# Kernel tuning notes

Measured on AMD Instinct MI355X. Metric: run time of the kernel, lower is better.

## Reference

```python
import jax, jax.numpy as jnp
import numpy as np

B, TT, TP, TO = 8, 128, 256, 512
V, D, H, L = 1024, 1024, 16, 12
FF = 4 * D
DH = D // H
EPS = 1e-5


def _pe(t, d):
    # sinusoidal PE: concat(sin(omega*t), cos(omega*t)), omega = exp(-ln(1e4)*i/(d/2))
    half = d // 2
    omega = jnp.exp(-jnp.log(10000.0) * jnp.arange(half, dtype=jnp.float32) / half)
    ang = jnp.arange(t, dtype=jnp.float32)[:, None] * omega[None, :]  # (t, d/2)
    return jnp.concatenate([jnp.sin(ang), jnp.cos(ang)], axis=-1)  # (t, d)


def _ln(x, g, b):
    mu = x.mean(axis=-1, keepdims=True)
    var = ((x - mu) ** 2).mean(axis=-1, keepdims=True)
    return (x - mu) / jnp.sqrt(var + EPS) * g + b


def _forward(text_ids, prompt_ids, output_ids, text_tab, prompt_tab, output_tab, sep,
             ln1_g, ln1_b, qkv_w, out_w, out_b, ln2_g, ln2_b,
             ff1_w, ff1_b, ff2_w, ff2_b, fc_w, fc_b):
    emb = lambda ids, tab: tab[ids] + _pe(ids.shape[1], D)[None]
    sep_tok = jnp.broadcast_to(sep, (B, 1, D))
    # join: [text, sep, prompt, sep, output]
    x = jnp.concatenate([emb(text_ids, text_tab), sep_tok,
                         emb(prompt_ids, prompt_tab), sep_tok,
                         emb(output_ids, output_tab)], axis=1)  # (B, T, D)
    T = x.shape[1]
    causal = jnp.tril(jnp.ones((T, T), dtype=bool))  # (T, T)
    scale = DH ** -0.5
    neg = -jnp.finfo(x.dtype).max
    for l in range(L):
        # attention block (prenorm residual); uniform lengths -> mask m is all ones
        h = _ln(x, ln1_g[l], ln1_b[l])
        qkv = h @ qkv_w[l]  # (B, T, 3D)
        q, k, v = jnp.split(qkv, 3, axis=-1)
        q = q.reshape(B, T, H, DH)
        k = k.reshape(B, T, H, DH)
        v = v.reshape(B, T, H, DH)
        e = jnp.einsum('bihd,bjhd->bijh', q, k) * scale
        e = jnp.where(causal[None, :, :, None], e, neg)
        a = jax.nn.softmax(e, axis=2)
        o = jnp.einsum('bijh,bjhd->bihd', a, v).reshape(B, T, D)
        x = x + o @ out_w[l] + out_b[l]
        # ffn block (prenorm residual), exact GELU as torch nn.GELU default
        h2 = _ln(x, ln2_g[l], ln2_b[l])
        ff = jax.nn.gelu(h2 @ ff1_w[l] + ff1_b[l], approximate=False) @ ff2_w[l] + ff2_b[l]
        x = x + ff
    h = x @ fc_w + fc_b  # (B, T, V)
    return h[:, -1, :]  # logits of last position, (B, V)


def setup_inputs() -> dict:
    key = jax.random.key(0)
    ks = iter(jax.random.split(key, 32))
    s = 0.02
    inp = {
        'text_ids': jax.random.randint(next(ks), (B, TT), 0, V),
        'prompt_ids': jax.random.randint(next(ks), (B, TP), 0, V),
        'output_ids': jax.random.randint(next(ks), (B, TO), 0, V),
        'text_tab': jax.random.normal(next(ks), (V, D), jnp.float32) * s,
        'prompt_tab': jax.random.normal(next(ks), (V, D), jnp.float32) * s,
        'output_tab': jax.random.normal(next(ks), (V, D), jnp.float32) * s,
        'sep': jax.random.normal(next(ks), (D,), jnp.float32),
        'ln1_g': jnp.ones((L, D), jnp.float32),
        'ln1_b': jnp.zeros((L, D), jnp.float32),
        'qkv_w': jax.random.normal(next(ks), (L, D, 3 * D), jnp.float32) * s,
        'out_w': jax.random.normal(next(ks), (L, D, D), jnp.float32) * s,
        'out_b': jnp.zeros((L, D), jnp.float32),
        'ln2_g': jnp.ones((L, D), jnp.float32),
        'ln2_b': jnp.zeros((L, D), jnp.float32),
        'ff1_w': jax.random.normal(next(ks), (L, D, FF), jnp.float32) * s,
        'ff1_b': jnp.zeros((L, FF), jnp.float32),
        'ff2_w': jax.random.normal(next(ks), (L, FF, D), jnp.float32) * s,
        'ff2_b': jnp.zeros((L, D), jnp.float32),
        'fc_w': jax.random.normal(next(ks), (D, V), jnp.float32) * s,
        'fc_b': jnp.zeros((V,), jnp.float32),
    }
    return inp


def reference(text_ids, prompt_ids, output_ids, text_tab, prompt_tab, output_tab, sep,
              ln1_g, ln1_b, qkv_w, out_w, out_b, ln2_g, ln2_b,
              ff1_w, ff1_b, ff2_w, ff2_b, fc_w, fc_b):
    return _forward(text_ids, prompt_ids, output_ids, text_tab, prompt_tab, output_tab, sep,
                    ln1_g, ln1_b, qkv_w, out_w, out_b, ln2_g, ln2_b,
                    ff1_w, ff1_b, ff2_w, ff2_b, fc_w, fc_b)
```

## Files before the change

### kernel.cpp

```cpp
#include <hip/hip_runtime.h>
#include <hip/hip_bf16.h>
#include <math.h>

#define Bn 8
#define Tn 898
#define Dn 1024
#define Hn 16
#define DHn 64
#define Ln 12
#define FFn 4096
#define Vn 1024
#define BT (Bn*Tn)

typedef short bf16x8 __attribute__((ext_vector_type(8)));
typedef float f32x4 __attribute__((ext_vector_type(4)));

__device__ __forceinline__ ushort f2bf(float f) {
    union { float f; unsigned u; } c; c.f = f;
    unsigned r = c.u + 0x7fffu + ((c.u >> 16) & 1u);
    return (ushort)(r >> 16);
}

__device__ __forceinline__ void glds16(const void* g, void* l) {
    __builtin_amdgcn_global_load_lds(
        (const __attribute__((address_space(1))) unsigned int*)g,
        (__attribute__((address_space(3))) unsigned int*)l, 16, 0, 0);
}

__global__ __launch_bounds__(256) void transpose_cast_kernel(
    const float* __restrict__ in, ushort* __restrict__ out,
    int K, int N, size_t in_ls, size_t out_ls)
{
    __shared__ ushort t[64][68];
    const float* inp = in + (size_t)blockIdx.z * in_ls;
    ushort* outp = out + (size_t)blockIdx.z * out_ls;
    int n0 = blockIdx.x * 64, k0 = blockIdx.y * 64;
    int tx = threadIdx.x & 63, ty = threadIdx.x >> 6;
    #pragma unroll
    for (int p = 0; p < 16; p++) {
        int kl = p * 4 + ty;
        t[tx][kl] = f2bf(inp[(size_t)(k0 + kl) * N + n0 + tx]);
    }
    __syncthreads();
    int tx4 = threadIdx.x & 15, ty4 = threadIdx.x >> 4;
    #pragma unroll
    for (int p = 0; p < 4; p++) {
        int nl = p * 16 + ty4;
        ushort4 v;
        v.x = t[nl][4*tx4]; v.y = t[nl][4*tx4+1]; v.z = t[nl][4*tx4+2]; v.w = t[nl][4*tx4+3];
        *(ushort4*)&outp[(size_t)(n0 + nl) * K + k0 + 4*tx4] = v;
    }
}

__global__ __launch_bounds__(256) void embed_kernel(
    const int* __restrict__ tids, const int* __restrict__ pids, const int* __restrict__ oids,
    const float* __restrict__ ttab, const float* __restrict__ ptab, const float* __restrict__ otab,
    const float* __restrict__ sep, float* __restrict__ x)
{
    int bp = blockIdx.x;
    int b = bp / Tn, pos = bp - b * Tn;
    int d0 = threadIdx.x * 4;
    float4 r;
    if (pos == 128 || pos == 385) {
        r = *(const float4*)(sep + d0);
    } else {
        int t; int id; const float* tab;
        if (pos < 128)      { t = pos;       id = tids[b*128 + t]; tab = ttab; }
        else if (pos < 385) { t = pos - 129; id = pids[b*256 + t]; tab = ptab; }
        else                { t = pos - 386; id = oids[b*512 + t]; tab = otab; }
        float4 e = *(const float4*)(tab + (size_t)id * Dn + d0);
        float pe[4];
        #pragma unroll
        for (int i = 0; i < 4; i++) {
            int d = d0 + i;
            int ii = d & 511;
            float omega = expf(-9.210340371976184f * (float)ii * (1.0f/512.0f));
            float ang = (float)t * omega;
            pe[i] = (d < 512) ? sinf(ang) : cosf(ang);
        }
        r.x = e.x + pe[0]; r.y = e.y + pe[1]; r.z = e.z + pe[2]; r.w = e.w + pe[3];
    }
    *(float4*)(x + (size_t)bp * Dn + d0) = r;
}

__global__ __launch_bounds__(256) void ln_kernel(
    const float* __restrict__ x, const float* __restrict__ g, const float* __restrict__ bt,
    ushort* __restrict__ out)
{
    __shared__ float red[8];
    int row = blockIdx.x, tid = threadIdx.x;
    float4 v = ((const float4*)(x + (size_t)row * Dn))[tid];
    float s = v.x + v.y + v.z + v.w;
    #pragma unroll
    for (int o = 32; o; o >>= 1) s += __shfl_down(s, o);
    if ((tid & 63) == 0) red[tid >> 6] = s;
    __syncthreads();
    float mu = (red[0] + red[1] + red[2] + red[3]) * (1.0f / Dn);
    float d0 = v.x - mu, d1 = v.y - mu, d2 = v.z - mu, d3 = v.w - mu;
    float s2 = d0*d0 + d1*d1 + d2*d2 + d3*d3;
    #pragma unroll
    for (int o = 32; o; o >>= 1) s2 += __shfl_down(s2, o);
    if ((tid & 63) == 0) red[4 + (tid >> 6)] = s2;
    __syncthreads();
    float var = (red[4] + red[5] + red[6] + red[7]) * (1.0f / Dn);
    float rstd = rsqrtf(var + 1e-5f);
    float4 gg = ((const float4*)g)[tid];
    float4 bb = ((const float4*)bt)[tid];
    ushort4 o4;
    o4.x = f2bf(d0 * rstd * gg.x + bb.x);
    o4.y = f2bf(d1 * rstd * gg.y + bb.y);
    o4.z = f2bf(d2 * rstd * gg.z + bb.z);
    o4.w = f2bf(d3 * rstd * gg.w + bb.w);
    ((ushort4*)(out + (size_t)row * Dn))[tid] = o4;
}

template<int BN, int MODE>
__global__ __launch_bounds__(256) void gemmk(
    const ushort* __restrict__ A, const ushort* __restrict__ Bw,
    const float* __restrict__ bias, const float* __restrict__ resid,
    void* __restrict__ Cout, int M, int N, int K, int nx)
{
    constexpr int NI = BN / 32;
    __shared__ ushort sA[128 * 32];
    __shared__ ushort sB[BN * 32];

    int tid = threadIdx.x, lane = tid & 63, wv = tid >> 6;
    int wm = wv >> 1, wn = wv & 1;
    int l16 = lane & 15, lhi = lane >> 4;

    int nb = gridDim.x, bid = blockIdx.x;
    int qq = nb >> 3, rr8 = nb & 7;
    int xcd = bid & 7, idx = bid >> 3;
    int wg = (xcd < rr8 ? xcd * (qq + 1) : rr8 * (qq + 1) + (xcd - rr8) * qq) + idx;
    int mt = wg / nx, ntt = wg - mt * nx;
    int m0 = mt * 128, n0 = ntt * BN;

    f32x4 acc[4][NI];
    #pragma unroll
    for (int i = 0; i < 4; i++)
        #pragma unroll
        for (int j = 0; j < NI; j++) acc[i][j] = (f32x4){0.f, 0.f, 0.f, 0.f};

    const size_t K2 = (size_t)K * 2;
    int srow = lane >> 2;
    int schk = ((lane & 3) ^ ((lane >> 3) & 3)) * 16;
    const char* Abase = (const char*)A + (size_t)m0 * K2 + schk;
    const char* Bbase = (const char*)Bw + (size_t)n0 * K2 + schk;

    auto stage = [&](int t) {
        size_t ko = (size_t)t * 64;
        glds16(Abase + (size_t)(wv * 16 + srow) * K2 + ko,       (char*)sA + wv * 1024);
        glds16(Abase + (size_t)((wv + 4) * 16 + srow) * K2 + ko, (char*)sA + (wv + 4) * 1024);
        glds16(Bbase + (size_t)(wv * 16 + srow) * K2 + ko,       (char*)sB + wv * 1024);
        if (BN == 128)
            glds16(Bbase + (size_t)((wv + 4) * 16 + srow) * K2 + ko, (char*)sB + (wv + 4) * 1024);
    };

    const int sc = (lhi ^ ((l16 >> 1) & 3)) * 8;
    auto compute = [&]() {
        bf16x8 af[4], bf[NI];
        #pragma unroll
        for (int mi = 0; mi < 4; mi++)
            af[mi] = *(const bf16x8*)&sA[(wm * 64 + mi * 16 + l16) * 32 + sc];
        #pragma unroll
        for (int ni = 0; ni < NI; ni++)
            bf[ni] = *(const bf16x8*)&sB[(wn * (16 * NI) + ni * 16 + l16) * 32 + sc];
        #pragma unroll
        for (int mi = 0; mi < 4; mi++)
            #pragma unroll
            for (int ni = 0; ni < NI; ni++)
                acc[mi][ni] = __builtin_amdgcn_mfma_f32_16x16x32_bf16(af[mi], bf[ni], acc[mi][ni], 0, 0, 0);
    };

    int ntile = K >> 5;
    for (int t = 0; t < ntile; ++t) {
        __syncthreads();
        stage(t);
        __syncthreads();
        compute();
    }

    #pragma unroll
    for (int mi = 0; mi < 4; mi++) {
        int rl = wm * 64 + mi * 16 + lhi * 4;
        #pragma unroll
        for (int ni = 0; ni < NI; ni++) {
            int gcol = n0 + wn * (16 * NI) + ni * 16 + l16;
            float bs = (MODE == 0) ? 0.0f : bias[gcol];
            #pragma unroll
            for (int j = 0; j < 4; j++) {
                int grow = m0 + rl + j;
                if (grow >= M) continue;
                float v = acc[mi][ni][j] + bs;
                if (MODE == 1) {
                    float rv = resid[(size_t)grow * N + gcol];
                    ((float*)Cout)[(size_t)grow * N + gcol] = rv + v;
                } else if (MODE == 2) {
                    float u = v * (1.5957691216f + 0.0713548163f * v * v);
                    float g = v / (1.0f + __expf(-u));
                    ((ushort*)Cout)[(size_t)grow * N + gcol] = f2bf(g);
                } else {
                    ((ushort*)Cout)[(size_t)grow * N + gcol] = f2bf(v);
                }
            }
        }
    }
}

__global__ __launch_bounds__(256) void attn_kernel(
    const ushort* __restrict__ qkv, ushort* __restrict__ out)
{
    __shared__ ushort Ksm[64 * 72];
    __shared__ ushort Vsm[64 * 72];
    __shared__ ushort Psm[4][16 * 72];
    int qt = blockIdx.x, b = blockIdx.y, h = blockIdx.z;
    int tid = threadIdx.x, lane = tid & 63, wave = tid >> 6;
    int l16 = lane & 15, lhi = lane >> 4;

    int qrow = qt*64 + wave*16 + l16;
    bf16x8 qf0 = {}, qf1 = {};
    if (qrow < Tn) {
        const ushort* qp = qkv + (size_t)(b*Tn + qrow) * 3072 + h*64 + lhi*8;
        qf0 = *(const bf16x8*)qp;
        qf1 = *(const bf16x8*)(qp + 32);
    }

    f32x4 o[4];
    #pragma unroll
    for (int i = 0; i < 4; i++) o[i] = (f32x4){0.f,0.f,0.f,0.f};
    float mrun[4] = {-1e30f,-1e30f,-1e30f,-1e30f};
    float sume[4] = {0.f,0.f,0.f,0.f};

    int kr = tid >> 2, cc = (tid & 3) * 16;
    const ushort* kvbase = qkv + (size_t)(b*Tn) * 3072 + h*64 + cc;
    int qg = qt*64 + wave*16 + lhi*4;

    for (int jt = 0; jt <= qt; jt++) {
        int kvr = jt*64 + kr;
        uint4 k0 = make_uint4(0,0,0,0), k1 = k0, v0 = k0, v1 = k0;
        if (kvr < Tn) {
            const ushort* p = kvbase + (size_t)kvr * 3072;
            k0 = *(const uint4*)(p + 1024);
            k1 = *(const uint4*)(p + 1024 + 8);
            v0 = *(const uint4*)(p + 2048);
            v1 = *(const uint4*)(p + 2048 + 8);
        }
        __syncthreads();
        *(uint4*)&Ksm[kr * 72 + cc] = k0;
        *(uint4*)&Ksm[kr * 72 + cc + 8] = k1;
        {
            ushort vv[16];
            *(uint4*)&vv[0] = v0; *(uint4*)&vv[8] = v1;
            #pragma unroll
            for (int i = 0; i < 16; i++) Vsm[(cc + i) * 72 + kr] = vv[i];
        }
        __syncthreads();

        f32x4 s[4];
        #pragma unroll
        for (int ni = 0; ni < 4; ni++) {
            s[ni] = (f32x4){0.f,0.f,0.f,0.f};
            bf16x8 kf0 = *(const bf16x8*)&Ksm[(ni*16 + l16) * 72 + lhi*8];
            bf16x8 kf1 = *(const bf16x8*)&Ksm[(ni*16 + l16) * 72 + lhi*8 + 32];
            s[ni] = __builtin_amdgcn_mfma_f32_16x16x32_bf16(qf0, kf0, s[ni], 0, 0, 0);
            s[ni] = __builtin_amdgcn_mfma_f32_16x16x32_bf16(qf1, kf1, s[ni], 0, 0, 0);
        }

        float pv[4][4];
        #pragma unroll
        for (int j = 0; j < 4; j++) {
            int qgj = qg + j;
            float mx = -1e30f;
            #pragma unroll
            for (int ni = 0; ni < 4; ni++) {
                int kvg = jt*64 + ni*16 + l16;
                float e = (kvg <= qgj && kvg < Tn) ? s[ni][j] * 0.125f : -1e30f;
                pv[ni][j] = e;
                mx = fmaxf(mx, e);
            }
            #pragma unroll
            for (int m = 1; m < 16; m <<= 1) mx = fmaxf(mx, __shfl_xor(mx, m));
            float mnew = fmaxf(mrun[j], mx);
            float fac = expf(mrun[j] - mnew);
            mrun[j] = mnew;
            float rs = 0.f;
            #pragma unroll
            for (int ni = 0; ni < 4; ni++) { pv[ni][j] = expf(pv[ni][j] - mnew); rs += pv[ni][j]; }
            #pragma unroll
            for (int m = 1; m < 16; m <<= 1) rs += __shfl_xor(rs, m);
            sume[j] = sume[j] * fac + rs;
            #pragma unroll
            for (int di = 0; di < 4; di++) o[di][j] *= fac;
        }

        #pragma unroll
        for (int j = 0; j < 4; j++)
            #pragma unroll
            for (int ni = 0; ni < 4; ni++)
                Psm[wave][(lhi*4 + j) * 72 + ni*16 + l16] = f2bf(pv[ni][j]);
        __syncthreads();

        bf16x8 pf0 = *(const bf16x8*)&Psm[wave][l16 * 72 + lhi*8];
        bf16x8 pf1 = *(const bf16x8*)&Psm[wave][l16 * 72 + lhi*8 + 32];
        #pragma unroll
        for (int di = 0; di < 4; di++) {
            bf16x8 vf0 = *(const bf16x8*)&Vsm[(di*16 + l16) * 72 + lhi*8];
            bf16x8 vf1 = *(const bf16x8*)&Vsm[(di*16 + l16) * 72 + lhi*8 + 32];
            o[di] = __builtin_amdgcn_mfma_f32_16x16x32_bf16(pf0, vf0, o[di], 0, 0, 0);
            o[di] = __builtin_amdgcn_mfma_f32_16x16x32_bf16(pf1, vf1, o[di], 0, 0, 0);
        }
    }

    #pragma unroll
    for (int j = 0; j < 4; j++) {
        int qgj = qg + j;
        if (qgj >= Tn) continue;
        float inv = 1.0f / sume[j];
        #pragma unroll
        for (int di = 0; di < 4; di++)
            out[(size_t)(b*Tn + qgj) * Dn + h*64 + di*16 + l16] = f2bf(o[di][j] * inv);
    }
}

__global__ __launch_bounds__(256) void fc_kernel(
    const float* __restrict__ x, const float* __restrict__ w,
    const float* __restrict__ bias, float* __restrict__ out)
{
    __shared__ float xs[Dn];
    int b = blockIdx.y;
    int v = blockIdx.x * 256 + threadIdx.x;
    float4 t = ((const float4*)(x + (size_t)(b*Tn + Tn - 1) * Dn))[threadIdx.x];
    ((float4*)xs)[threadIdx.x] = t;
    __syncthreads();
    float acc = bias[v];
    for (int d = 0; d < Dn; d++)
        acc = fmaf(xs[d], w[(size_t)d * Vn + v], acc);
    out[(size_t)b * Vn + v] = acc;
}

extern "C" void kernel_launch(void* const* d_in, const int* in_sizes, int n_in,
                              void* d_out, int out_size, void* d_ws, size_t ws_size,
                              hipStream_t stream)
{
    const int*   text_ids  = (const int*)d_in[0];
    const int*   prompt_ids= (const int*)d_in[1];
    const int*   output_ids= (const int*)d_in[2];
    const float* text_tab  = (const float*)d_in[3];
    const float* prompt_tab= (const float*)d_in[4];
    const float* output_tab= (const float*)d_in[5];
    const float* sep       = (const float*)d_in[6];
    const float* ln1_g     = (const float*)d_in[7];
    const float* ln1_b     = (const float*)d_in[8];
    const float* qkv_w     = (const float*)d_in[9];
    const float* out_w     = (const float*)d_in[10];
    const float* out_b     = (const float*)d_in[11];
    const float* ln2_g     = (const float*)d_in[12];
    const float* ln2_b     = (const float*)d_in[13];
    const float* ff1_w     = (const float*)d_in[14];
    const float* ff1_b     = (const float*)d_in[15];
    const float* ff2_w     = (const float*)d_in[16];
    const float* ff2_b     = (const float*)d_in[17];
    const float* fc_w      = (const float*)d_in[18];
    const float* fc_b      = (const float*)d_in[19];

    char* ws = (char*)d_ws;
    float*  x    = (float*)(ws);
    ushort* h    = (ushort*)(ws + 29425664);
    ushort* qkv  = (ushort*)(ws + 44630016);
    ushort* attn = (ushort*)(ws + 90243072);
    ushort* ff1o = (ushort*)(ws + 105447424);
    ushort* wT   = (ushort*)(ws + 166264832);

    const size_t L_STRIDE = 12582912;
    const size_t OFF_QKV = 0, OFF_OUT = 3145728, OFF_FF1 = 4194304, OFF_FF2 = 8388608;
    const size_t upfront_need = 166264832ULL + 2ULL * L_STRIDE * Ln;
    const bool upfront = ws_size >= upfront_need;

    if (upfront) {
        transpose_cast_kernel<<<dim3(48,16,Ln), 256, 0, stream>>>(qkv_w, wT + OFF_QKV, Dn, 3*Dn, (size_t)Dn*3*Dn, L_STRIDE);
        transpose_cast_kernel<<<dim3(16,16,Ln), 256, 0, stream>>>(out_w, wT + OFF_OUT, Dn, Dn,   (size_t)Dn*Dn,   L_STRIDE);
        transpose_cast_kernel<<<dim3(64,16,Ln), 256, 0, stream>>>(ff1_w, wT + OFF_FF1, Dn, FFn,  (size_t)Dn*FFn,  L_STRIDE);
        transpose_cast_kernel<<<dim3(16,64,Ln), 256, 0, stream>>>(ff2_w, wT + OFF_FF2, FFn, Dn,  (size_t)FFn*Dn,  L_STRIDE);
    }

    embed_kernel<<<BT, 256, 0, stream>>>(text_ids, prompt_ids, output_ids,
                                         text_tab, prompt_tab, output_tab, sep, x);

    for (int l = 0; l < Ln; l++) {
        ushort* wb = upfront ? (wT + (size_t)l * L_STRIDE) : wT;
        if (!upfront) {
            transpose_cast_kernel<<<dim3(48,16,1), 256, 0, stream>>>(qkv_w + (size_t)l*Dn*3*Dn, wb + OFF_QKV, Dn, 3*Dn, 0, 0);
            transpose_cast_kernel<<<dim3(16,16,1), 256, 0, stream>>>(out_w + (size_t)l*Dn*Dn,   wb + OFF_OUT, Dn, Dn,   0, 0);
            transpose_cast_kernel<<<dim3(64,16,1), 256, 0, stream>>>(ff1_w + (size_t)l*Dn*FFn,  wb + OFF_FF1, Dn, FFn,  0, 0);
            transpose_cast_kernel<<<dim3(16,64,1), 256, 0, stream>>>(ff2_w + (size_t)l*FFn*Dn,  wb + OFF_FF2, FFn, Dn,  0, 0);
        }
        ln_kernel<<<BT, 256, 0, stream>>>(x, ln1_g + l*Dn, ln1_b + l*Dn, h);
        gemmk<128,0><<<57*24, 256, 0, stream>>>(
            h, wb + OFF_QKV, nullptr, nullptr, qkv, BT, 3*Dn, Dn, 24);
        attn_kernel<<<dim3(15, Bn, Hn), 256, 0, stream>>>(qkv, attn);
        gemmk<64,1><<<57*16, 256, 0, stream>>>(
            attn, wb + OFF_OUT, out_b + l*Dn, x, x, BT, Dn, Dn, 16);
        ln_kernel<<<BT, 256, 0, stream>>>(x, ln2_g + l*Dn, ln2_b + l*Dn, h);
        gemmk<128,2><<<57*32, 256, 0, stream>>>(
            h, wb + OFF_FF1, ff1_b + l*FFn, nullptr, ff1o, BT, FFn, Dn, 32);
        gemmk<64,1><<<57*16, 256, 0, stream>>>(
            ff1o, wb + OFF_FF2, ff2_b + l*Dn, x, x, BT, Dn, FFn, 16);
    }

    fc_kernel<<<dim3(Vn/256, Bn), 256, 0, stream>>>(x, fc_w, fc_b, (float*)d_out);
}
```

Measured before the change: 5.360 ms.

## Double-buffer GEMM LDS staging and use one wavefront per row in layernorm

The GEMM now keeps two LDS buffers and issues the global-to-LDS loads for the next K-tile before computing the current one. This replaces two barriers per tile with a single vmcnt wait plus barrier, so load latency can overlap MFMA work, at the cost of twice the shared memory per block. The layernorm kernel now gives each row to one 64-lane wavefront and reduces with xor shuffles, which removes the shared-memory reductions and block barriers and launches a quarter as many blocks. BT is divisible by 4, so all rows are still covered.

```diff
diff --git a/kernel.cpp b/kernel.cpp
--- a/kernel.cpp
+++ b/kernel.cpp
@@ -26,6 +26,9 @@
         (const __attribute__((address_space(1))) unsigned int*)g,
         (__attribute__((address_space(3))) unsigned int*)l, 16, 0, 0);
 }
+
+#define BARRIER() __builtin_amdgcn_s_barrier()
+#define VMCNT0() asm volatile("s_waitcnt vmcnt(0)" ::: "memory")
 
 __global__ __launch_bounds__(256) void transpose_cast_kernel(
     const float* __restrict__ in, ushort* __restrict__ out,
@@ -87,31 +90,40 @@
     const float* __restrict__ x, const float* __restrict__ g, const float* __restrict__ bt,
     ushort* __restrict__ out)
 {
-    __shared__ float red[8];
-    int row = blockIdx.x, tid = threadIdx.x;
-    float4 v = ((const float4*)(x + (size_t)row * Dn))[tid];
-    float s = v.x + v.y + v.z + v.w;
-    #pragma unroll
-    for (int o = 32; o; o >>= 1) s += __shfl_down(s, o);
-    if ((tid & 63) == 0) red[tid >> 6] = s;
-    __syncthreads();
-    float mu = (red[0] + red[1] + red[2] + red[3]) * (1.0f / Dn);
-    float d0 = v.x - mu, d1 = v.y - mu, d2 = v.z - mu, d3 = v.w - mu;
-    float s2 = d0*d0 + d1*d1 + d2*d2 + d3*d3;
-    #pragma unroll
-    for (int o = 32; o; o >>= 1) s2 += __shfl_down(s2, o);
-    if ((tid & 63) == 0) red[4 + (tid >> 6)] = s2;
-    __syncthreads();
-    float var = (red[4] + red[5] + red[6] + red[7]) * (1.0f / Dn);
-    float rstd = rsqrtf(var + 1e-5f);
-    float4 gg = ((const float4*)g)[tid];
-    float4 bb = ((const float4*)bt)[tid];
-    ushort4 o4;
-    o4.x = f2bf(d0 * rstd * gg.x + bb.x);
-    o4.y = f2bf(d1 * rstd * gg.y + bb.y);
-    o4.z = f2bf(d2 * rstd * gg.z + bb.z);
-    o4.w = f2bf(d3 * rstd * gg.w + bb.w);
-    ((ushort4*)(out + (size_t)row * Dn))[tid] = o4;
+    int row = blockIdx.x * 4 + (threadIdx.x >> 6);
+    int lane = threadIdx.x & 63;
+    const float4* xr = (const float4*)(x + (size_t)row * Dn);
+    float4 v[4];
+    float s = 0.f;
+    #pragma unroll
+    for (int i = 0; i < 4; i++) {
+        v[i] = xr[lane + 64 * i];
+        s += v[i].x + v[i].y + v[i].z + v[i].w;
+    }
+    #pragma unroll
+    for (int o = 32; o; o >>= 1) s += __shfl_xor(s, o);
+    float mu = s * (1.0f / Dn);
+    float s2 = 0.f;
+    #pragma unroll
+    for (int i = 0; i < 4; i++) {
+        v[i].x -= mu; v[i].y -= mu; v[i].z -= mu; v[i].w -= mu;
+        s2 += v[i].x*v[i].x + v[i].y*v[i].y + v[i].z*v[i].z + v[i].w*v[i].w;
+    }
+    #pragma unroll
+    for (int o = 32; o; o >>= 1) s2 += __shfl_xor(s2, o);
+    float rstd = rsqrtf(s2 * (1.0f / Dn) + 1e-5f);
+    ushort4* orow = (ushort4*)(out + (size_t)row * Dn);
+    #pragma unroll
+    for (int i = 0; i < 4; i++) {
+        float4 gg = ((const float4*)g)[lane + 64 * i];
+        float4 bb = ((const float4*)bt)[lane + 64 * i];
+        ushort4 o4;
+        o4.x = f2bf(v[i].x * rstd * gg.x + bb.x);
+        o4.y = f2bf(v[i].y * rstd * gg.y + bb.y);
+        o4.z = f2bf(v[i].z * rstd * gg.z + bb.z);
+        o4.w = f2bf(v[i].w * rstd * gg.w + bb.w);
+        orow[lane + 64 * i] = o4;
+    }
 }
 
 template<int BN, int MODE>
@@ -121,8 +133,8 @@
     void* __restrict__ Cout, int M, int N, int K, int nx)
 {
     constexpr int NI = BN / 32;
-    __shared__ ushort sA[128 * 32];
-    __shared__ ushort sB[BN * 32];
+    __shared__ ushort sA[2][128 * 32];
+    __shared__ ushort sB[2][BN * 32];
 
     int tid = threadIdx.x, lane = tid & 63, wv = tid >> 6;
     int wm = wv >> 1, wn = wv & 1;
@@ -144,27 +156,30 @@
     const size_t K2 = (size_t)K * 2;
     int srow = lane >> 2;
     int schk = ((lane & 3) ^ ((lane >> 3) & 3)) * 16;
-    const char* Abase = (const char*)A + (size_t)m0 * K2 + schk;
-    const char* Bbase = (const char*)Bw + (size_t)n0 * K2 + schk;
-
-    auto stage = [&](int t) {
-        size_t ko = (size_t)t * 64;
-        glds16(Abase + (size_t)(wv * 16 + srow) * K2 + ko,       (char*)sA + wv * 1024);
-        glds16(Abase + (size_t)((wv + 4) * 16 + srow) * K2 + ko, (char*)sA + (wv + 4) * 1024);
-        glds16(Bbase + (size_t)(wv * 16 + srow) * K2 + ko,       (char*)sB + wv * 1024);
+    const char* Aw0 = (const char*)A + (size_t)(m0 + wv * 16 + srow) * K2 + schk;
+    const char* Aw1 = (const char*)A + (size_t)(m0 + (wv + 4) * 16 + srow) * K2 + schk;
+    const char* Bp0 = (const char*)Bw + (size_t)(n0 + wv * 16 + srow) * K2 + schk;
+    const char* Bp1 = (BN == 128) ? (const char*)Bw + (size_t)(n0 + (wv + 4) * 16 + srow) * K2 + schk : nullptr;
+
+    auto stage = [&](int buf) {
+        glds16(Aw0, (char*)sA[buf] + wv * 1024);
+        glds16(Aw1, (char*)sA[buf] + (wv + 4) * 1024);
+        glds16(Bp0, (char*)sB[buf] + wv * 1024);
         if (BN == 128)
-            glds16(Bbase + (size_t)((wv + 4) * 16 + srow) * K2 + ko, (char*)sB + (wv + 4) * 1024);
+            glds16(Bp1, (char*)sB[buf] + (wv + 4) * 1024);
+        Aw0 += 64; Aw1 += 64; Bp0 += 64;
+        if (BN == 128) Bp1 += 64;
     };
 
     const int sc = (lhi ^ ((l16 >> 1) & 3)) * 8;
-    auto compute = [&]() {
+    auto compute = [&](int buf) {
         bf16x8 af[4], bf[NI];
         #pragma unroll
         for (int mi = 0; mi < 4; mi++)
-            af[mi] = *(const bf16x8*)&sA[(wm * 64 + mi * 16 + l16) * 32 + sc];
+            af[mi] = *(const bf16x8*)&sA[buf][(wm * 64 + mi * 16 + l16) * 32 + sc];
         #pragma unroll
         for (int ni = 0; ni < NI; ni++)
-            bf[ni] = *(const bf16x8*)&sB[(wn * (16 * NI) + ni * 16 + l16) * 32 + sc];
+            bf[ni] = *(const bf16x8*)&sB[buf][(wn * (16 * NI) + ni * 16 + l16) * 32 + sc];
         #pragma unroll
         for (int mi = 0; mi < 4; mi++)
             #pragma unroll
@@ -173,11 +188,16 @@
     };
 
     int ntile = K >> 5;
+    stage(0);
+    VMCNT0();
+    BARRIER();
+    int cur = 0;
     for (int t = 0; t < ntile; ++t) {
-        __syncthreads();
-        stage(t);
-        __syncthreads();
-        compute();
+        if (t + 1 < ntile) stage(cur ^ 1);
+        compute(cur);
+        VMCNT0();
+        BARRIER();
+        cur ^= 1;
     }
 
     #pragma unroll
@@ -394,13 +414,13 @@
             transpose_cast_kernel<<<dim3(64,16,1), 256, 0, stream>>>(ff1_w + (size_t)l*Dn*FFn,  wb + OFF_FF1, Dn, FFn,  0, 0);
             transpose_cast_kernel<<<dim3(16,64,1), 256, 0, stream>>>(ff2_w + (size_t)l*FFn*Dn,  wb + OFF_FF2, FFn, Dn,  0, 0);
         }
-        ln_kernel<<<BT, 256, 0, stream>>>(x, ln1_g + l*Dn, ln1_b + l*Dn, h);
+        ln_kernel<<<BT/4, 256, 0, stream>>>(x, ln1_g + l*Dn, ln1_b + l*Dn, h);
         gemmk<128,0><<<57*24, 256, 0, stream>>>(
             h, wb + OFF_QKV, nullptr, nullptr, qkv, BT, 3*Dn, Dn, 24);
         attn_kernel<<<dim3(15, Bn, Hn), 256, 0, stream>>>(qkv, attn);
         gemmk<64,1><<<57*16, 256, 0, stream>>>(
             attn, wb + OFF_OUT, out_b + l*Dn, x, x, BT, Dn, Dn, 16);
-        ln_kernel<<<BT, 256, 0, stream>>>(x, ln2_g + l*Dn, ln2_b + l*Dn, h);
+        ln_kernel<<<BT/4, 256, 0, stream>>>(x, ln2_g + l*Dn, ln2_b + l*Dn, h);
         gemmk<128,2><<<57*32, 256, 0, stream>>>(
             h, wb + OFF_FF1, ff1_b + l*FFn, nullptr, ff1o, BT, FFn, Dn, 32);
         gemmk<64,1><<<57*16, 256, 0, stream>>>(
```

New measurement: 5.144 ms. 4.0% less time.
